# Kernel optimization log

Measured on AMD Instinct MI355X. Metric: run time of the kernel, lower is better.

Reference implementation:

```python
import jax, jax.numpy as jnp
import numpy as np

ALPHA = 0.2  # LeakyReLU negative slope
NEG = -1e10  # mask value, matches -10000000000.0


def _gat_head(feat, adj, W, a1, a2):
    # feat: [N, Fin], W: [Fin, Fout], a1/a2: [Fout]
    h = feat @ W                              # [N, Fout]
    s = h @ a1                                # [N] attn_for_self
    t = h @ a2                                # [N] attn_for_neighs
    logits = jax.nn.leaky_relu(s[:, None] + t[None, :], ALPHA)  # [N, N]
    logits = logits + NEG * (1.0 - adj)       # additive adjacency mask
    attn = jax.nn.softmax(logits, axis=-1)    # [N, N]
    return attn @ h                           # [N, Fout]


def setup_inputs() -> dict:
    key = jax.random.key(0)
    ks = jax.random.split(key, 9)
    N, NFEAT, NHID, NCLASS, H = 6144, 128, 64, 16, 4
    glorot = jax.nn.initializers.glorot_uniform()
    adj = (jax.random.uniform(ks[0], (N, N)) < 0.005).astype(jnp.float32)
    feature = jax.random.normal(ks[1], (N, NFEAT), dtype=jnp.float32)
    in0 = NFEAT * H
    W0 = jnp.stack([glorot(ks[2 + i], (in0, NHID), jnp.float32) for i in range(H)])  # [H,in0,NHID]
    a1_0 = jax.random.normal(ks[6], (H, NHID), dtype=jnp.float32) * 0.1
    a2_0 = jax.random.normal(ks[7], (H, NHID), dtype=jnp.float32) * 0.1
    Wout = glorot(ks[8], (NHID * H, NCLASS), jnp.float32)
    a1_out = jax.random.normal(jax.random.fold_in(key, 100), (NCLASS,), dtype=jnp.float32) * 0.1
    a2_out = jax.random.normal(jax.random.fold_in(key, 101), (NCLASS,), dtype=jnp.float32) * 0.1
    return {"adj": adj, "feature": feature, "W0": W0, "a1_0": a1_0, "a2_0": a2_0,
            "Wout": Wout, "a1_out": a1_out, "a2_out": a2_out}


def reference(adj, feature, W0, a1_0, a2_0, Wout, a1_out, a2_out):
    H = W0.shape[0]
    N = feature.shape[0]
    x = jnp.tile(feature, (1, H))  # [N, nfeat*H]
    # hidden layer: H heads, concat=True -> elu then concat along features
    heads = jax.vmap(_gat_head, in_axes=(None, None, 0, 0, 0))(x, adj, W0, a1_0, a2_0)  # [H,N,NHID]
    heads = jax.nn.elu(heads)
    x = jnp.transpose(heads, (1, 0, 2)).reshape(N, -1)  # [N, H*NHID]
    # output layer: concat=False (no elu inside), then elu + softmax in GAT.call
    out = _gat_head(x, adj, Wout, a1_out, a2_out)  # [N, nclass]
    out = jax.nn.elu(out)
    return jax.nn.softmax(out, axis=-1)
```

## Files before the change

### kernel.cpp

```cpp
#include <hip/hip_runtime.h>
#include <cstdint>
#include <math.h>

#define N 6144
#define FIN 128
#define FH 64
#define NHEADS 4
#define NC 16
#define CAP 512
#define ALPHA 0.2f
#define NT 16

__device__ __forceinline__ float wave_sum(float v) {
    #pragma unroll
    for (int off = 32; off >= 1; off >>= 1) v += __shfl_xor(v, off);
    return v;
}
__device__ __forceinline__ float wave_max(float v) {
    #pragma unroll
    for (int off = 32; off >= 1; off >>= 1) v = fmaxf(v, __shfl_xor(v, off));
    return v;
}

__global__ void k_hgemm(const float* __restrict__ feat, const float* __restrict__ W0,
                        const float* __restrict__ a1, const float* __restrict__ a2,
                        float* __restrict__ hfeat, float* __restrict__ sb,
                        float* __restrict__ tb) {
    __shared__ float fl[NT * FIN];
    int tid = threadIdx.x;
    int n0 = blockIdx.x * NT;
    for (int idx = tid; idx < NT * FIN; idx += 256) fl[idx] = feat[(size_t)n0 * FIN + idx];
    __syncthreads();
    int f = tid & 63, h = tid >> 6;
    const float* w0 = W0 + (size_t)h * 512 * 64 + f;
    float acc[NT];
    #pragma unroll
    for (int nn = 0; nn < NT; nn++) acc[nn] = 0.f;
    for (int k = 0; k < FIN; k++) {
        float w = w0[(size_t)k * 64] + w0[(size_t)(128 + k) * 64]
                + w0[(size_t)(256 + k) * 64] + w0[(size_t)(384 + k) * 64];
        #pragma unroll
        for (int nn = 0; nn < NT; nn++) acc[nn] = fmaf(fl[nn * FIN + k], w, acc[nn]);
    }
    float a1v = a1[h * FH + f], a2v = a2[h * FH + f];
    #pragma unroll
    for (int nn = 0; nn < NT; nn++) {
        hfeat[((size_t)h * N + (n0 + nn)) * FH + f] = acc[nn];
        float s = wave_sum(acc[nn] * a1v);
        float t = wave_sum(acc[nn] * a2v);
        if ((tid & 63) == 0) { sb[h * N + n0 + nn] = s; tb[h * N + n0 + nn] = t; }
    }
}

__global__ void k_row(const float* __restrict__ adj, const float* __restrict__ hfeat,
                      const float* __restrict__ sb, const float* __restrict__ tb,
                      const float* __restrict__ wout, const float* __restrict__ a1o,
                      const float* __restrict__ a2o,
                      int* __restrict__ cols, int* __restrict__ deg,
                      float* __restrict__ h2, float* __restrict__ s2,
                      float* __restrict__ t2) {
    int i = blockIdx.x;
    int tid = threadIdx.x;
    int lane = tid & 63, h = tid >> 6;
    __shared__ int lidx[CAP];
    __shared__ float xrow[NHEADS * FH];
    __shared__ int wtot[4];

    const float4* rowv = (const float4*)(adj + (size_t)i * N);
    float4 rv[6];
    #pragma unroll
    for (int it = 0; it < 6; it++) rv[it] = rowv[it * 256 + tid];

    unsigned int bits = 0;
    int c = 0;
    #pragma unroll
    for (int it = 0; it < 6; it++) {
        bool p0 = rv[it].x != 0.f, p1 = rv[it].y != 0.f;
        bool p2 = rv[it].z != 0.f, p3 = rv[it].w != 0.f;
        bits |= (unsigned)p0 << (it * 4 + 0);
        bits |= (unsigned)p1 << (it * 4 + 1);
        bits |= (unsigned)p2 << (it * 4 + 2);
        bits |= (unsigned)p3 << (it * 4 + 3);
        c += (int)p0 + (int)p1 + (int)p2 + (int)p3;
    }
    int inc = c;
    #pragma unroll
    for (int off = 1; off < 64; off <<= 1) {
        int v = __shfl_up(inc, off);
        if (lane >= off) inc += v;
    }
    if (lane == 63) wtot[h] = inc;
    __syncthreads();
    int wbase = 0;
    #pragma unroll
    for (int w = 0; w < 4; w++) wbase += (w < h) ? wtot[w] : 0;
    int d = wtot[0] + wtot[1] + wtot[2] + wtot[3];
    int base = wbase + inc - c;
    #pragma unroll
    for (int it = 0; it < 6; it++) {
        #pragma unroll
        for (int cc = 0; cc < 4; cc++) {
            if (bits & (1u << (it * 4 + cc))) {
                if (base < CAP) lidx[base] = (it * 256 + tid) * 4 + cc;
                base++;
            }
        }
    }
    __syncthreads();
    if (tid == 0) deg[i] = d;
    for (int t = tid; t < min(d, CAP); t += 256) cols[(size_t)i * CAP + t] = lidx[t];

    int mode = (d == 0) ? 1 : (d > CAP ? 2 : 0);
    int count = (mode == 0) ? d : N;
    const float* trow = tb + (size_t)h * N;
    const float* hrow = hfeat + (size_t)h * N * FH;
    float si = sb[h * N + i];
    int q = lane >> 4, fo = (lane & 15) * 4;
    float m = -INFINITY, l = 0.f;
    float4 acc = {0.f, 0.f, 0.f, 0.f};
    for (int bs = 0; bs < count; bs += 64) {
        int idx = bs + lane;
        int j = 0; float lr = -INFINITY;
        if (idx < count) {
            j = (mode == 0) ? lidx[idx] : idx;
            bool ok = (mode != 2) || (adj[(size_t)i * N + j] != 0.f);
            if (ok) {
                float z = si + trow[j];
                lr = (z >= 0.f) ? z : ALPHA * z;
            }
        }
        float mc = wave_max(lr);
        float mn = fmaxf(m, mc);
        if (mn == -INFINITY) continue;
        float scale = (m == -INFINITY) ? 0.f : expf(m - mn);
        float w = (lr == -INFINITY) ? 0.f : expf(lr - mn);
        l = l * scale + wave_sum(w);
        acc.x *= scale; acc.y *= scale; acc.z *= scale; acc.w *= scale;
        int cn = min(64, count - bs);
        #pragma unroll 4
        for (int bb = 0; bb < cn; bb += 4) {
            float wb = __shfl(w, bb + q);
            int jn = __shfl(j, bb + q);
            float4 hv = *(const float4*)(hrow + (size_t)jn * FH + fo);
            acc.x = fmaf(wb, hv.x, acc.x);
            acc.y = fmaf(wb, hv.y, acc.y);
            acc.z = fmaf(wb, hv.z, acc.z);
            acc.w = fmaf(wb, hv.w, acc.w);
        }
        m = mn;
    }
    #pragma unroll
    for (int off = 16; off <= 32; off <<= 1) {
        acc.x += __shfl_xor(acc.x, off);
        acc.y += __shfl_xor(acc.y, off);
        acc.z += __shfl_xor(acc.z, off);
        acc.w += __shfl_xor(acc.w, off);
    }
    if (lane < 16) {
        float linv = 1.f / l;
        float4 o;
        o.x = acc.x * linv; o.y = acc.y * linv; o.z = acc.z * linv; o.w = acc.w * linv;
        o.x = (o.x > 0.f) ? o.x : expm1f(o.x);
        o.y = (o.y > 0.f) ? o.y : expm1f(o.y);
        o.z = (o.z > 0.f) ? o.z : expm1f(o.z);
        o.w = (o.w > 0.f) ? o.w : expm1f(o.w);
        *(float4*)(xrow + h * FH + fo) = o;
    }
    __syncthreads();

    if (h == 0) {
        int f = lane & 15, part = lane >> 4;
        float dot = 0.f;
        #pragma unroll
        for (int k = 0; k < 64; k++)
            dot = fmaf(xrow[part * 64 + k], wout[(size_t)(part * 64 + k) * NC + f], dot);
        dot += __shfl_xor(dot, 16);
        dot += __shfl_xor(dot, 32);
        if (lane < NC) h2[(size_t)i * NC + lane] = dot;
        float sv = (lane < NC) ? dot * a1o[lane] : 0.f;
        float tv = (lane < NC) ? dot * a2o[lane] : 0.f;
        sv = wave_sum(sv); tv = wave_sum(tv);
        if (lane == 0) { s2[i] = sv; t2[i] = tv; }
    }
}

__global__ void k_attn_out(const float* __restrict__ h2, const float* __restrict__ s2,
                           const float* __restrict__ t2, const int* __restrict__ cols,
                           const int* __restrict__ deg, const float* __restrict__ adj,
                           float* __restrict__ out) {
    int w = threadIdx.x >> 6, lane = threadIdx.x & 63;
    int i = blockIdx.x * 4 + w;
    int d = deg[i];
    int mode = (d == 0) ? 1 : (d > CAP ? 2 : 0);
    int count = (mode == 0) ? d : N;
    const int* crow = cols + (size_t)i * CAP;
    float si = s2[i];
    int f = lane & 15, q = lane >> 4;
    float m = -INFINITY, l = 0.f, acc = 0.f;
    for (int bs = 0; bs < count; bs += 64) {
        int idx = bs + lane;
        int j = 0; float lr = -INFINITY;
        if (idx < count) {
            j = (mode == 0) ? crow[idx] : idx;
            bool ok = (mode != 2) || (adj[(size_t)i * N + j] != 0.f);
            if (ok) {
                float z = si + t2[j];
                lr = (z >= 0.f) ? z : ALPHA * z;
            }
        }
        float mc = wave_max(lr);
        float mn = fmaxf(m, mc);
        if (mn == -INFINITY) continue;
        float scale = (m == -INFINITY) ? 0.f : expf(m - mn);
        float wv = (lr == -INFINITY) ? 0.f : expf(lr - mn);
        l = l * scale + wave_sum(wv);
        acc *= scale;
        int cn = min(64, count - bs);
        #pragma unroll 4
        for (int bb = 0; bb < cn; bb += 4) {
            float wb = __shfl(wv, bb + q);
            int jn = __shfl(j, bb + q);
            acc = fmaf(wb, h2[(size_t)jn * NC + f], acc);
        }
        m = mn;
    }
    acc += __shfl_xor(acc, 16);
    acc += __shfl_xor(acc, 32);
    float o = acc / l;
    o = (o > 0.f) ? o : expm1f(o);
    float mv = (lane < NC) ? o : -INFINITY;
    float mx = wave_max(mv);
    float e = (lane < NC) ? expf(o - mx) : 0.f;
    float se = wave_sum(e);
    if (lane < NC) out[(size_t)i * NC + lane] = e / se;
}

extern "C" void kernel_launch(void* const* d_in, const int* in_sizes, int n_in,
                              void* d_out, int out_size, void* d_ws, size_t ws_size,
                              hipStream_t stream) {
    const float* adj  = (const float*)d_in[0];
    const float* feat = (const float*)d_in[1];
    const float* W0   = (const float*)d_in[2];
    const float* a1_0 = (const float*)d_in[3];
    const float* a2_0 = (const float*)d_in[4];
    const float* Wout = (const float*)d_in[5];
    const float* a1o  = (const float*)d_in[6];
    const float* a2o  = (const float*)d_in[7];
    float* outp = (float*)d_out;

    float* hfeat = (float*)d_ws;
    float* sb    = hfeat + 1572864;
    float* tb    = sb + 24576;
    float* h2    = tb + 24576;
    float* s2    = h2 + 98304;
    float* t2    = s2 + 6144;
    int*   cols  = (int*)(t2 + 6144);
    int*   deg   = cols + (size_t)N * CAP;

    k_hgemm<<<N / NT, 256, 0, stream>>>(feat, W0, a1_0, a2_0, hfeat, sb, tb);
    k_row<<<N, 256, 0, stream>>>(adj, hfeat, sb, tb, Wout, a1o, a2o,
                                 cols, deg, h2, s2, t2);
    k_attn_out<<<N / 4, 256, 0, stream>>>(h2, s2, t2, cols, deg, adj, outp);
}
```

Before: 284.9 us.

## Overlap adjacency compaction with feature GEMM in a merged front kernel

Moves the adjacency-row scan and neighbor compaction out of the row-attention kernel into a combined front kernel. Blocks there either run the head GEMM or compact one adjacency row using ballot plus shared-atomic prefix, so the 150MB adjacency read overlaps the GEMM instead of waiting behind it. It also halves the GEMM row tile and batches weight loads in chunks of 8. The aggregation kernel now reloads the compacted indices from global memory. Because of the atomic, neighbor order within a row becomes nondeterministic, which can change floating-point summation order.

```diff
diff --git a/kernel.cpp b/kernel.cpp
--- a/kernel.cpp
+++ b/kernel.cpp
@@ -9,7 +9,8 @@
 #define NC 16
 #define CAP 512
 #define ALPHA 0.2f
-#define NT 16
+#define NT 8
+#define NGEMM (N / NT)
 
 __device__ __forceinline__ float wave_sum(float v) {
     #pragma unroll
@@ -22,93 +23,96 @@
     return v;
 }
 
-__global__ void k_hgemm(const float* __restrict__ feat, const float* __restrict__ W0,
-                        const float* __restrict__ a1, const float* __restrict__ a2,
+__global__ void k_front(const float* __restrict__ adj, const float* __restrict__ feat,
+                        const float* __restrict__ W0, const float* __restrict__ a1,
+                        const float* __restrict__ a2,
                         float* __restrict__ hfeat, float* __restrict__ sb,
-                        float* __restrict__ tb) {
+                        float* __restrict__ tb,
+                        int* __restrict__ cols, int* __restrict__ deg) {
     __shared__ float fl[NT * FIN];
-    int tid = threadIdx.x;
-    int n0 = blockIdx.x * NT;
-    for (int idx = tid; idx < NT * FIN; idx += 256) fl[idx] = feat[(size_t)n0 * FIN + idx];
-    __syncthreads();
-    int f = tid & 63, h = tid >> 6;
-    const float* w0 = W0 + (size_t)h * 512 * 64 + f;
-    float acc[NT];
-    #pragma unroll
-    for (int nn = 0; nn < NT; nn++) acc[nn] = 0.f;
-    for (int k = 0; k < FIN; k++) {
-        float w = w0[(size_t)k * 64] + w0[(size_t)(128 + k) * 64]
-                + w0[(size_t)(256 + k) * 64] + w0[(size_t)(384 + k) * 64];
-        #pragma unroll
-        for (int nn = 0; nn < NT; nn++) acc[nn] = fmaf(fl[nn * FIN + k], w, acc[nn]);
-    }
-    float a1v = a1[h * FH + f], a2v = a2[h * FH + f];
-    #pragma unroll
-    for (int nn = 0; nn < NT; nn++) {
-        hfeat[((size_t)h * N + (n0 + nn)) * FH + f] = acc[nn];
-        float s = wave_sum(acc[nn] * a1v);
-        float t = wave_sum(acc[nn] * a2v);
-        if ((tid & 63) == 0) { sb[h * N + n0 + nn] = s; tb[h * N + n0 + nn] = t; }
-    }
-}
-
-__global__ void k_row(const float* __restrict__ adj, const float* __restrict__ hfeat,
+    int* lidx = (int*)fl;
+    __shared__ int cnt;
+    int tid = threadIdx.x, lane = tid & 63, h = tid >> 6;
+
+    if (blockIdx.x < NGEMM) {
+        int n0 = blockIdx.x * NT;
+        for (int idx = tid; idx < NT * FIN; idx += 256)
+            fl[idx] = feat[(size_t)n0 * FIN + idx];
+        __syncthreads();
+        const float* w0 = W0 + (size_t)h * 512 * 64 + lane;
+        float acc[NT];
+        #pragma unroll
+        for (int nn = 0; nn < NT; nn++) acc[nn] = 0.f;
+        for (int kc = 0; kc < FIN; kc += 8) {
+            float wch[8];
+            #pragma unroll
+            for (int kk = 0; kk < 8; kk++) {
+                int k = kc + kk;
+                wch[kk] = w0[(size_t)k * 64] + w0[(size_t)(128 + k) * 64]
+                        + w0[(size_t)(256 + k) * 64] + w0[(size_t)(384 + k) * 64];
+            }
+            #pragma unroll
+            for (int kk = 0; kk < 8; kk++)
+                #pragma unroll
+                for (int nn = 0; nn < NT; nn++)
+                    acc[nn] = fmaf(fl[nn * FIN + kc + kk], wch[kk], acc[nn]);
+        }
+        float a1v = a1[h * FH + lane], a2v = a2[h * FH + lane];
+        #pragma unroll
+        for (int nn = 0; nn < NT; nn++) {
+            hfeat[((size_t)h * N + (n0 + nn)) * FH + lane] = acc[nn];
+            float s = wave_sum(acc[nn] * a1v);
+            float t = wave_sum(acc[nn] * a2v);
+            if (lane == 0) { sb[h * N + n0 + nn] = s; tb[h * N + n0 + nn] = t; }
+        }
+    } else {
+        int i = blockIdx.x - NGEMM;
+        if (tid == 0) cnt = 0;
+        __syncthreads();
+        const float4* rowv = (const float4*)(adj + (size_t)i * N);
+        float4 rv[6];
+        #pragma unroll
+        for (int it = 0; it < 6; it++) rv[it] = rowv[it * 256 + tid];
+        unsigned long long lmask = (1ull << lane) - 1ull;
+        #pragma unroll
+        for (int it = 0; it < 6; it++) {
+            int jb = (it * 256 + tid) * 4;
+            bool p[4] = {rv[it].x != 0.f, rv[it].y != 0.f, rv[it].z != 0.f, rv[it].w != 0.f};
+            #pragma unroll
+            for (int c = 0; c < 4; c++) {
+                unsigned long long mm = __ballot(p[c]);
+                int tot = __popcll(mm);
+                if (tot) {
+                    int prefix = __popcll(mm & lmask);
+                    int wb;
+                    if (lane == 0) wb = atomicAdd(&cnt, tot);
+                    wb = __shfl(wb, 0);
+                    int pos = wb + prefix;
+                    if (p[c] && pos < CAP) lidx[pos] = jb + c;
+                }
+            }
+        }
+        __syncthreads();
+        int d = cnt;
+        if (tid == 0) deg[i] = d;
+        for (int t = tid; t < min(d, CAP); t += 256) cols[(size_t)i * CAP + t] = lidx[t];
+    }
+}
+
+__global__ void k_agg(const float* __restrict__ adj, const float* __restrict__ hfeat,
                       const float* __restrict__ sb, const float* __restrict__ tb,
                       const float* __restrict__ wout, const float* __restrict__ a1o,
                       const float* __restrict__ a2o,
-                      int* __restrict__ cols, int* __restrict__ deg,
+                      const int* __restrict__ cols, const int* __restrict__ deg,
                       float* __restrict__ h2, float* __restrict__ s2,
                       float* __restrict__ t2) {
     int i = blockIdx.x;
-    int tid = threadIdx.x;
-    int lane = tid & 63, h = tid >> 6;
+    int tid = threadIdx.x, lane = tid & 63, h = tid >> 6;
     __shared__ int lidx[CAP];
     __shared__ float xrow[NHEADS * FH];
-    __shared__ int wtot[4];
-
-    const float4* rowv = (const float4*)(adj + (size_t)i * N);
-    float4 rv[6];
-    #pragma unroll
-    for (int it = 0; it < 6; it++) rv[it] = rowv[it * 256 + tid];
-
-    unsigned int bits = 0;
-    int c = 0;
-    #pragma unroll
-    for (int it = 0; it < 6; it++) {
-        bool p0 = rv[it].x != 0.f, p1 = rv[it].y != 0.f;
-        bool p2 = rv[it].z != 0.f, p3 = rv[it].w != 0.f;
-        bits |= (unsigned)p0 << (it * 4 + 0);
-        bits |= (unsigned)p1 << (it * 4 + 1);
-        bits |= (unsigned)p2 << (it * 4 + 2);
-        bits |= (unsigned)p3 << (it * 4 + 3);
-        c += (int)p0 + (int)p1 + (int)p2 + (int)p3;
-    }
-    int inc = c;
-    #pragma unroll
-    for (int off = 1; off < 64; off <<= 1) {
-        int v = __shfl_up(inc, off);
-        if (lane >= off) inc += v;
-    }
-    if (lane == 63) wtot[h] = inc;
+    int d = deg[i];
+    for (int t = tid; t < min(d, CAP); t += 256) lidx[t] = cols[(size_t)i * CAP + t];
     __syncthreads();
-    int wbase = 0;
-    #pragma unroll
-    for (int w = 0; w < 4; w++) wbase += (w < h) ? wtot[w] : 0;
-    int d = wtot[0] + wtot[1] + wtot[2] + wtot[3];
-    int base = wbase + inc - c;
-    #pragma unroll
-    for (int it = 0; it < 6; it++) {
-        #pragma unroll
-        for (int cc = 0; cc < 4; cc++) {
-            if (bits & (1u << (it * 4 + cc))) {
-                if (base < CAP) lidx[base] = (it * 256 + tid) * 4 + cc;
-                base++;
-            }
-        }
-    }
-    __syncthreads();
-    if (tid == 0) deg[i] = d;
-    for (int t = tid; t < min(d, CAP); t += 256) cols[(size_t)i * CAP + t] = lidx[t];
 
     int mode = (d == 0) ? 1 : (d > CAP ? 2 : 0);
     int count = (mode == 0) ? d : N;
@@ -257,8 +261,9 @@
     int*   cols  = (int*)(t2 + 6144);
     int*   deg   = cols + (size_t)N * CAP;
 
-    k_hgemm<<<N / NT, 256, 0, stream>>>(feat, W0, a1_0, a2_0, hfeat, sb, tb);
-    k_row<<<N, 256, 0, stream>>>(adj, hfeat, sb, tb, Wout, a1o, a2o,
+    k_front<<<NGEMM + N, 256, 0, stream>>>(adj, feat, W0, a1_0, a2_0,
+                                           hfeat, sb, tb, cols, deg);
+    k_agg<<<N, 256, 0, stream>>>(adj, hfeat, sb, tb, Wout, a1o, a2o,
                                  cols, deg, h2, s2, t2);
     k_attn_out<<<N / 4, 256, 0, stream>>>(h2, s2, t2, cols, deg, adj, outp);
 }
```

Result: no change. 279.6 us (-1.8%).
